# Optimization experiments

Hardware: AMD Instinct MI355X
Metric: run time of the kernel (lower is better)

## Reference

```python
import jax, jax.numpy as jnp
import numpy as np

POS_LEN = 19
SEQ = POS_LEN * POS_LEN
C = 768
H = 12
HD = C // H  # 64
FFN = 2048
L = 8
EPS = 1e-6


def make_rope():
    # 2D rotary embedding over the 19x19 board, half the freq dims for rows, half for cols.
    d_half = HD // 2          # 32
    quarter = d_half // 2     # 16
    inv_freq = 1.0 / (10000.0 ** (jnp.arange(quarter, dtype=jnp.float32) / quarter))
    pos = jnp.arange(POS_LEN, dtype=jnp.float32)
    rows = jnp.repeat(pos, POS_LEN)   # [SEQ]
    cols = jnp.tile(pos, POS_LEN)     # [SEQ]
    ang_r = rows[:, None] * inv_freq[None, :]  # [SEQ, quarter]
    ang_c = cols[:, None] * inv_freq[None, :]  # [SEQ, quarter]
    emb = jnp.concatenate([ang_r, ang_c], axis=-1)      # [SEQ, HD//2]
    emb = jnp.concatenate([emb, emb], axis=-1)          # [SEQ, HD]
    return jnp.cos(emb), jnp.sin(emb)


def rmsnorm(x, gamma):
    var = jnp.mean(jnp.square(x), axis=-1, keepdims=True)
    return x * jax.lax.rsqrt(var + EPS) * gamma


def rotate_half(x):
    a, b = jnp.split(x, 2, axis=-1)
    return jnp.concatenate([-b, a], axis=-1)


def apply_rope(x, cos, sin):
    # x: [B,S,H,HD], cos/sin: [S,HD]
    return x * cos[None, :, None, :] + rotate_half(x) * sin[None, :, None, :]


def setup_inputs() -> dict:
    key = jax.random.key(0)
    ks = jax.random.split(key, 10)
    s = 0.02
    inp = {
        "input_spatial": jax.random.normal(ks[0], (32, 22, POS_LEN, POS_LEN), jnp.float32),
        "input_global": jax.random.normal(ks[1], (32, 19), jnp.float32),
        "conv_w": jax.random.normal(ks[2], (C, 22, 3, 3), jnp.float32) * s,
        "Wg": jax.random.normal(ks[3], (19, C), jnp.float32) * s,
        "qkv_gamma": jnp.ones((L, C), jnp.float32),
        "Wqkv": jax.random.normal(ks[4], (L, C, 3 * C), jnp.float32) * s,
        "Wproj": jax.random.normal(ks[5], (L, C, C), jnp.float32) * s,
        "mlp_gamma": jnp.ones((L, C), jnp.float32),
        "Wfc1": jax.random.normal(ks[6], (L, C, 2 * FFN), jnp.float32) * s,
        "Wfc2": jax.random.normal(ks[7], (L, FFN, C), jnp.float32) * s,
        "final_gamma": jnp.ones((C,), jnp.float32),
    }
    return inp


def reference(input_spatial, input_global, conv_w, Wg, qkv_gamma, Wqkv, Wproj,
              mlp_gamma, Wfc1, Wfc2, final_gamma):
    B = input_spatial.shape[0]
    cos, sin = make_rope()
    # Stem: conv over spatial planes + broadcast global linear
    x_sp = jax.lax.conv_general_dilated(
        input_spatial, conv_w, window_strides=(1, 1), padding="SAME",
        dimension_numbers=("NCHW", "OIHW", "NCHW"))           # [B,C,19,19]
    x_g = input_global @ Wg                                       # [B,C]
    x = x_sp + x_g[:, :, None, None]
    x = x.reshape(B, C, SEQ).transpose(0, 2, 1)                   # [B,S,C]

    scale = 1.0 / jnp.sqrt(jnp.float32(HD))
    for i in range(L):
        # RMSNorm + QKV
        h = rmsnorm(x, qkv_gamma[i])
        qkv = (h @ Wqkv[i]).reshape(B, SEQ, 3, H, HD)
        q, k, v = qkv[:, :, 0], qkv[:, :, 1], qkv[:, :, 2]        # [B,S,H,HD]
        q = apply_rope(q, cos, sin)
        k = apply_rope(k, cos, sin)
        # Attention (no mask)
        scores = jnp.einsum("bshd,bthd->bhst", q, k) * scale      # [B,H,S,S]
        attn = jax.nn.softmax(scores, axis=-1)
        o = jnp.einsum("bhst,bthd->bshd", attn, v).reshape(B, SEQ, C)
        x = x + o @ Wproj[i]
        # RMSNorm + SwiGLU MLP
        h = rmsnorm(x, mlp_gamma[i])
        u = h @ Wfc1[i]                                           # [B,S,2*FFN]
        a, b = jnp.split(u, 2, axis=-1)
        x = x + (jax.nn.silu(a) * b) @ Wfc2[i]

    return rmsnorm(x, final_gamma).astype(jnp.float32)
```

## Files before the change

kernel.cpp:

```cpp
#include <hip/hip_runtime.h>
#include <hip/hip_bf16.h>
#include <math.h>

#define B_    32
#define SEQ_  361
#define C_    768
#define H_    12
#define HD_   64
#define FFN_  2048
#define L_    8
#define M_    (B_*SEQ_)
#define MPAD_ 11648
#define MBLK_ (MPAD_/128)

typedef _Float16 f16;
typedef f16  f16x8 __attribute__((ext_vector_type(8)));
typedef float f32x4 __attribute__((ext_vector_type(4)));

__global__ void bias_kernel(const float* __restrict__ inG, const float* __restrict__ Wg,
                            float* __restrict__ bias) {
  int idx = blockIdx.x * blockDim.x + threadIdx.x;
  if (idx >= B_ * C_) return;
  int b = idx / C_, c = idx - b * C_;
  float acc = 0.f;
  #pragma unroll
  for (int j = 0; j < 19; ++j) acc += inG[b * 19 + j] * Wg[j * C_ + c];
  bias[idx] = acc;
}

__global__ void rope_table_kernel(float* __restrict__ cost, float* __restrict__ sint) {
  int idx = blockIdx.x * blockDim.x + threadIdx.x;
  if (idx >= SEQ_ * 32) return;
  int s = idx / 32, j = idx - s * 32;
  float row = (float)(s / 19), col = (float)(s % 19);
  int q = (j < 16) ? j : (j - 16);
  float invf = powf(10000.f, -(float)q / 16.f);
  float ang = ((j < 16) ? row : col) * invf;
  float cv = cosf(ang), sv = sinf(ang);
  cost[s * 64 + j] = cv; cost[s * 64 + j + 32] = cv;
  sint[s * 64 + j] = sv; sint[s * 64 + j + 32] = sv;
}

__global__ __launch_bounds__(256) void conv_kernel(const float* __restrict__ inS,
    const float* __restrict__ convW, const float* __restrict__ bias,
    float* __restrict__ X) {
  __shared__ float in_l[22][441];
  __shared__ float w_l[24][198];
  int b = blockIdx.x;
  int cb = blockIdx.y * 24;
  int tid = threadIdx.x;
  for (int i = tid; i < 22 * 441; i += 256) (&in_l[0][0])[i] = 0.f;
  __syncthreads();
  for (int i = tid; i < 22 * 361; i += 256) {
    int ci = i / 361, s = i - ci * 361, r = s / 19, c = s - r * 19;
    in_l[ci][(r + 1) * 21 + (c + 1)] = inS[(size_t)(b * 22 + ci) * 361 + s];
  }
  for (int i = tid; i < 24 * 198; i += 256)
    (&w_l[0][0])[i] = convW[(size_t)cb * 198 + i];
  __syncthreads();
  for (int o = tid; o < 24 * 361; o += 256) {
    int col = o / 361, s = o - col * 361, r = s / 19, c = s - r * 19;
    float acc = bias[b * C_ + cb + col];
    const float* wr = &w_l[col][0];
    #pragma unroll
    for (int ci = 0; ci < 22; ++ci) {
      const float* ib = &in_l[ci][r * 21 + c];
      const float* wp = wr + ci * 9;
      acc += wp[0]*ib[0]  + wp[1]*ib[1]  + wp[2]*ib[2]
           + wp[3]*ib[21] + wp[4]*ib[22] + wp[5]*ib[23]
           + wp[6]*ib[42] + wp[7]*ib[43] + wp[8]*ib[44];
    }
    X[(size_t)(b * SEQ_ + s) * C_ + cb + col] = acc;
  }
}

__global__ __launch_bounds__(256) void wcvt_kernel(const float* __restrict__ W,
    f16* __restrict__ WT, int K, int N) {
  __shared__ float t[32][33];
  int n0 = blockIdx.x * 32, k0 = blockIdx.y * 32;
  size_t base = (size_t)blockIdx.z * K * N;
  int c = threadIdx.x & 31, r = threadIdx.x >> 5;
  #pragma unroll
  for (int rr = 0; rr < 32; rr += 8)
    t[r + rr][c] = W[base + (size_t)(k0 + r + rr) * N + n0 + c];
  __syncthreads();
  #pragma unroll
  for (int rr = 0; rr < 32; rr += 8)
    WT[base + (size_t)(n0 + r + rr) * K + k0 + c] = (f16)t[c][r + rr];
}

template<bool F16OUT>
__global__ __launch_bounds__(256) void rmsnorm_kernel(const float* __restrict__ X,
    const float* __restrict__ gamma, void* __restrict__ Out) {
  int row = blockIdx.x;
  const float* xp = X + (size_t)row * C_;
  int t = threadIdx.x;
  float v0 = xp[t], v1 = xp[t + 256], v2 = xp[t + 512];
  float ss = v0 * v0 + v1 * v1 + v2 * v2;
  #pragma unroll
  for (int off = 32; off > 0; off >>= 1) ss += __shfl_down(ss, off);
  __shared__ float ws4[4];
  if ((t & 63) == 0) ws4[t >> 6] = ss;
  __syncthreads();
  float tot = ws4[0] + ws4[1] + ws4[2] + ws4[3];
  float r = 1.0f / sqrtf(tot * (1.f / 768.f) + 1e-6f);
  if (F16OUT) {
    f16* op = (f16*)Out + (size_t)row * C_;
    op[t]       = (f16)(v0 * r * gamma[t]);
    op[t + 256] = (f16)(v1 * r * gamma[t + 256]);
    op[t + 512] = (f16)(v2 * r * gamma[t + 512]);
  } else {
    float* op = (float*)Out + (size_t)row * C_;
    op[t]       = v0 * r * gamma[t];
    op[t + 256] = v1 * r * gamma[t + 256];
    op[t + 512] = v2 * r * gamma[t + 512];
  }
}

template<int MODE>
__global__ __launch_bounds__(256, 2) void hgemm(const f16* __restrict__ A,
    const f16* __restrict__ BT, void* __restrict__ Cout, int N, int K) {
  __shared__ f16 As[128 * 32];
  __shared__ f16 Bs[128 * 32];
  int tid = threadIdx.x;
  int w = tid >> 6, lane = tid & 63, lo = lane & 15, hi = lane >> 4;
  int bm = blockIdx.y * 128, bn = blockIdx.x * 128;
  int wr = (w >> 1) * 64, wc = (w & 1) * 64;
  f32x4 acc[4][4] = {};
  f16x8 ra[2], rb[2];
  const f16* Abase = A  + (size_t)bm * K;
  const f16* Bbase = BT + (size_t)bn * K;

  auto loadT = [&](int kt) {
    #pragma unroll
    for (int c = 0; c < 2; ++c) {
      int id = c * 256 + tid;
      ra[c] = *(const f16x8*)(Abase + (size_t)(id >> 2) * K + kt + (id & 3) * 8);
      rb[c] = *(const f16x8*)(Bbase + (size_t)(id >> 2) * K + kt + (id & 3) * 8);
    }
  };
  auto writeT = [&]() {
    #pragma unroll
    for (int c = 0; c < 2; ++c) {
      int id = c * 256 + tid;
      int row = id >> 2, ch = id & 3;
      int off = row * 32 + ((ch ^ ((row >> 1) & 3)) << 3);
      *(f16x8*)(As + off) = ra[c];
      *(f16x8*)(Bs + off) = rb[c];
    }
  };

  loadT(0);
  for (int kt = 0; kt < K; kt += 32) {
    writeT();
    __syncthreads();
    if (kt + 32 < K) loadT(kt + 32);
    f16x8 af[4], bf[4];
    #pragma unroll
    for (int m = 0; m < 4; ++m) {
      int row = wr + m * 16 + lo;
      af[m] = *(const f16x8*)(As + row * 32 + ((hi ^ ((row >> 1) & 3)) << 3));
    }
    #pragma unroll
    for (int n = 0; n < 4; ++n) {
      int row = wc + n * 16 + lo;
      bf[n] = *(const f16x8*)(Bs + row * 32 + ((hi ^ ((row >> 1) & 3)) << 3));
    }
    #pragma unroll
    for (int m = 0; m < 4; ++m)
      #pragma unroll
      for (int n = 0; n < 4; ++n)
        acc[m][n] = __builtin_amdgcn_mfma_f32_16x16x32_f16(af[m], bf[n], acc[m][n], 0, 0, 0);
    __syncthreads();
  }

  #pragma unroll
  for (int m = 0; m < 4; ++m) {
    #pragma unroll
    for (int n = 0; n < 4; ++n) {
      #pragma unroll
      for (int r = 0; r < 4; ++r) {
        size_t off = (size_t)(bm + wr + m * 16 + hi * 4 + r) * N + bn + wc + n * 16 + lo;
        if (MODE == 0) {
          ((f16*)Cout)[off] = (f16)acc[m][n][r];
        } else {
          float* O = (float*)Cout;
          O[off] = O[off] + acc[m][n][r];
        }
      }
    }
  }
}

__global__ __launch_bounds__(256, 2) void hgemm_gate(const f16* __restrict__ A,
    const f16* __restrict__ BT, f16* __restrict__ G) {
  const int K = C_;
  __shared__ f16 As[128 * 32];
  __shared__ f16 Bs0[64 * 32];
  __shared__ f16 Bs1[64 * 32];
  int tid = threadIdx.x;
  int w = tid >> 6, lane = tid & 63, lo = lane & 15, hi = lane >> 4;
  int bm = blockIdx.y * 128, bn = blockIdx.x * 64;
  int wr = (w >> 1) * 64, wc = (w & 1) * 32;
  f32x4 accA[4][2] = {}, accB[4][2] = {};
  f16x8 ra[2], rb0, rb1;
  const f16* Abase  = A + (size_t)bm * K;
  const f16* B0base = BT + (size_t)bn * K;
  const f16* B1base = BT + (size_t)(2048 + bn) * K;

  auto loadT = [&](int kt) {
    #pragma unroll
    for (int c = 0; c < 2; ++c) {
      int id = c * 256 + tid;
      ra[c] = *(const f16x8*)(Abase + (size_t)(id >> 2) * K + kt + (id & 3) * 8);
    }
    rb0 = *(const f16x8*)(B0base + (size_t)(tid >> 2) * K + kt + (tid & 3) * 8);
    rb1 = *(const f16x8*)(B1base + (size_t)(tid >> 2) * K + kt + (tid & 3) * 8);
  };
  auto writeT = [&]() {
    #pragma unroll
    for (int c = 0; c < 2; ++c) {
      int id = c * 256 + tid;
      int row = id >> 2, ch = id & 3;
      *(f16x8*)(As + row * 32 + ((ch ^ ((row >> 1) & 3)) << 3)) = ra[c];
    }
    int row = tid >> 2, ch = tid & 3;
    int off = row * 32 + ((ch ^ ((row >> 1) & 3)) << 3);
    *(f16x8*)(Bs0 + off) = rb0;
    *(f16x8*)(Bs1 + off) = rb1;
  };

  loadT(0);
  for (int kt = 0; kt < K; kt += 32) {
    writeT();
    __syncthreads();
    if (kt + 32 < K) loadT(kt + 32);
    f16x8 af[4], b0f[2], b1f[2];
    #pragma unroll
    for (int m = 0; m < 4; ++m) {
      int row = wr + m * 16 + lo;
      af[m] = *(const f16x8*)(As + row * 32 + ((hi ^ ((row >> 1) & 3)) << 3));
    }
    #pragma unroll
    for (int n = 0; n < 2; ++n) {
      int row = wc + n * 16 + lo;
      int off = row * 32 + ((hi ^ ((row >> 1) & 3)) << 3);
      b0f[n] = *(const f16x8*)(Bs0 + off);
      b1f[n] = *(const f16x8*)(Bs1 + off);
    }
    #pragma unroll
    for (int m = 0; m < 4; ++m)
      #pragma unroll
      for (int n = 0; n < 2; ++n) {
        accA[m][n] = __builtin_amdgcn_mfma_f32_16x16x32_f16(af[m], b0f[n], accA[m][n], 0, 0, 0);
        accB[m][n] = __builtin_amdgcn_mfma_f32_16x16x32_f16(af[m], b1f[n], accB[m][n], 0, 0, 0);
      }
    __syncthreads();
  }

  #pragma unroll
  for (int m = 0; m < 4; ++m)
    #pragma unroll
    for (int n = 0; n < 2; ++n)
      #pragma unroll
      for (int r = 0; r < 4; ++r) {
        float a = accA[m][n][r], bb = accB[m][n][r];
        float g = a / (1.f + expf(-a)) * bb;
        G[(size_t)(bm + wr + m * 16 + hi * 4 + r) * 2048 + bn + wc + n * 16 + lo] = (f16)g;
      }
}

__global__ void rope_apply_kernel(f16* __restrict__ qkv,
    const float* __restrict__ cost, const float* __restrict__ sint) {
  int idx = blockIdx.x * blockDim.x + threadIdx.x;
  const int total = M_ * 2 * H_ * 32;
  if (idx >= total) return;
  int d = idx & 31;
  int rest = idx >> 5;
  int h = rest % H_; rest /= H_;
  int which = rest & 1; rest >>= 1;
  int s = rest % SEQ_;
  int b = rest / SEQ_;
  size_t base = (size_t)(b * SEQ_ + s) * (3 * C_) + which * C_ + h * 64;
  float a  = (float)qkv[base + d];
  float bb = (float)qkv[base + d + 32];
  float cv = cost[s * 64 + d], sv = sint[s * 64 + d];
  qkv[base + d]      = (f16)(a * cv - bb * sv);
  qkv[base + d + 32] = (f16)(bb * cv + a * sv);
}

__global__ __launch_bounds__(256, 2) void attn_kernel(const f16* __restrict__ qkv,
                                                      f16* __restrict__ Out) {
  __shared__ f16 Kl[64 * 64];
  __shared__ f16 Vt[64 * 72];
  __shared__ f16 Pl[4][16 * 72];
  int tid = threadIdx.x;
  int w = tid >> 6, lane = tid & 63, lo = lane & 15, hi = lane >> 4;
  int qt = blockIdx.x, h = blockIdx.y, b = blockIdx.z;
  int q0 = qt * 64 + w * 16;
  const int RS = 3 * C_;

  f16x8 qf[2];
  {
    int qrow = q0 + lo; if (qrow > 360) qrow = 360;
    const f16* qp = qkv + (size_t)(b * SEQ_ + qrow) * RS + h * 64 + hi * 8;
    qf[0] = *(const f16x8*)(qp);
    qf[1] = *(const f16x8*)(qp + 32);
  }
  f32x4 o[4] = {};
  float mrun[4], lrun[4];
  #pragma unroll
  for (int r = 0; r < 4; ++r) { mrun[r] = -INFINITY; lrun[r] = 0.f; }

  for (int kt = 0; kt < SEQ_; kt += 64) {
    #pragma unroll
    for (int c = 0; c < 2; ++c) {
      int id = c * 256 + tid;
      {
        int row = id >> 3, ch = id & 7;
        int key = kt + row; if (key > 360) key = 360;
        f16x8 kv = *(const f16x8*)(qkv + (size_t)(b * SEQ_ + key) * RS + C_ + h * 64 + ch * 8);
        *(f16x8*)(Kl + row * 64 + ((ch ^ (row & 7)) << 3)) = kv;
      }
      {
        int kk = id & 63, d0 = (id >> 6) * 8;
        int key = kt + kk; if (key > 360) key = 360;
        f16x8 vv = *(const f16x8*)(qkv + (size_t)(b * SEQ_ + key) * RS + 2 * C_ + h * 64 + d0);
        #pragma unroll
        for (int j = 0; j < 8; ++j) Vt[(d0 + j) * 72 + kk] = vv[j];
      }
    }
    __syncthreads();

    f32x4 s[4] = {};
    #pragma unroll
    for (int f = 0; f < 4; ++f) {
      int row = f * 16 + lo;
      f16x8 k0 = *(const f16x8*)(Kl + row * 64 + ((hi ^ (row & 7)) << 3));
      f16x8 k1 = *(const f16x8*)(Kl + row * 64 + (((hi + 4) ^ (row & 7)) << 3));
      s[f] = __builtin_amdgcn_mfma_f32_16x16x32_f16(qf[0], k0, s[f], 0, 0, 0);
      s[f] = __builtin_amdgcn_mfma_f32_16x16x32_f16(qf[1], k1, s[f], 0, 0, 0);
    }
    float tmax[4] = {-INFINITY, -INFINITY, -INFINITY, -INFINITY};
    #pragma unroll
    for (int f = 0; f < 4; ++f) {
      bool ok = (kt + f * 16 + lo) < SEQ_;
      #pragma unroll
      for (int r = 0; r < 4; ++r) {
        float v = ok ? s[f][r] * 0.125f : -INFINITY;
        s[f][r] = v;
        tmax[r] = fmaxf(tmax[r], v);
      }
    }
    #pragma unroll
    for (int r = 0; r < 4; ++r) {
      #pragma unroll
      for (int mk = 1; mk < 16; mk <<= 1) tmax[r] = fmaxf(tmax[r], __shfl_xor(tmax[r], mk));
    }
    float rsc[4], psum[4] = {0.f, 0.f, 0.f, 0.f};
    #pragma unroll
    for (int r = 0; r < 4; ++r) {
      float mn = fmaxf(mrun[r], tmax[r]);
      rsc[r] = expf(mrun[r] - mn);
      mrun[r] = mn;
    }
    #pragma unroll
    for (int f = 0; f < 4; ++f)
      #pragma unroll
      for (int r = 0; r < 4; ++r) {
        float p = expf(s[f][r] - mrun[r]);
        s[f][r] = p;
        psum[r] += p;
      }
    #pragma unroll
    for (int r = 0; r < 4; ++r) {
      #pragma unroll
      for (int mk = 1; mk < 16; mk <<= 1) psum[r] += __shfl_xor(psum[r], mk);
      lrun[r] = lrun[r] * rsc[r] + psum[r];
    }
    #pragma unroll
    for (int n = 0; n < 4; ++n)
      #pragma unroll
      for (int r = 0; r < 4; ++r) o[n][r] *= rsc[r];
    f16* P = &Pl[w][0];
    #pragma unroll
    for (int f = 0; f < 4; ++f)
      #pragma unroll
      for (int r = 0; r < 4; ++r)
        P[(hi * 4 + r) * 72 + f * 16 + lo] = (f16)s[f][r];
    #pragma unroll
    for (int ks = 0; ks < 2; ++ks) {
      f16x8 pa = *(const f16x8*)(P + lo * 72 + hi * 8 + ks * 32);
      #pragma unroll
      for (int n = 0; n < 4; ++n) {
        f16x8 vf = *(const f16x8*)(Vt + (n * 16 + lo) * 72 + hi * 8 + ks * 32);
        o[n] = __builtin_amdgcn_mfma_f32_16x16x32_f16(pa, vf, o[n], 0, 0, 0);
      }
    }
    __syncthreads();
  }

  #pragma unroll
  for (int r = 0; r < 4; ++r) {
    int row = q0 + hi * 4 + r;
    if (row < SEQ_) {
      float inv = 1.f / lrun[r];
      #pragma unroll
      for (int n = 0; n < 4; ++n)
        Out[(size_t)(b * SEQ_ + row) * C_ + h * 64 + n * 16 + lo] = (f16)(o[n][r] * inv);
    }
  }
}

extern "C" void kernel_launch(void* const* d_in, const int* in_sizes, int n_in,
                              void* d_out, int out_size, void* d_ws, size_t ws_size,
                              hipStream_t stream) {
  (void)in_sizes; (void)n_in; (void)out_size;
  const float* inS   = (const float*)d_in[0];
  const float* inG   = (const float*)d_in[1];
  const float* convW = (const float*)d_in[2];
  const float* Wg    = (const float*)d_in[3];
  const float* qg    = (const float*)d_in[4];
  const float* Wqkv  = (const float*)d_in[5];
  const float* Wproj = (const float*)d_in[6];
  const float* mg    = (const float*)d_in[7];
  const float* Wfc1  = (const float*)d_in[8];
  const float* Wfc2  = (const float*)d_in[9];
  const float* fg    = (const float*)d_in[10];
  float* out = (float*)d_out;

  char* p = (char*)d_ws;
  float* x    = (float*)p;            p += (size_t)MPAD_ * C_ * 4;
  float* bias = (float*)p;            p += (size_t)B_ * C_ * 4;
  float* cost = (float*)p;            p += (size_t)SEQ_ * 64 * 4;
  float* sint = (float*)p;            p += (size_t)SEQ_ * 64 * 4;
  f16*   h16  = (f16*)p;              p += (size_t)MPAD_ * C_ * 2;
  f16*   qkv16= (f16*)p;              p += (size_t)MPAD_ * 3 * C_ * 2;
  f16*   g16  = qkv16;

  const size_t sq = (size_t)3 * C_ * C_;
  const size_t sp = (size_t)C_ * C_;
  const size_t s1 = (size_t)2 * FFN_ * C_;
  const size_t s2 = (size_t)C_ * FFN_;
  const size_t per_layer = sq + sp + s1 + s2;
  size_t used_common = (size_t)(p - (char*)d_ws);
  bool upfront = ws_size >= used_common + per_layer * L_ * 2 + 1024;
  size_t mult = upfront ? (size_t)L_ : 1;
  f16* wq  = (f16*)p;
  f16* wpj = wq  + sq * mult;
  f16* w1  = wpj + sp * mult;
  f16* w2  = w1  + s1 * mult;

  bias_kernel<<<dim3((B_ * C_ + 255) / 256), 256, 0, stream>>>(inG, Wg, bias);
  rope_table_kernel<<<dim3((SEQ_ * 32 + 255) / 256), 256, 0, stream>>>(cost, sint);
  conv_kernel<<<dim3(B_, 32), 256, 0, stream>>>(inS, convW, bias, x);

  if (upfront) {
    wcvt_kernel<<<dim3(3 * C_ / 32, C_ / 32, L_), 256, 0, stream>>>(Wqkv, wq, C_, 3 * C_);
    wcvt_kernel<<<dim3(C_ / 32, C_ / 32, L_), 256, 0, stream>>>(Wproj, wpj, C_, C_);
    wcvt_kernel<<<dim3(2 * FFN_ / 32, C_ / 32, L_), 256, 0, stream>>>(Wfc1, w1, C_, 2 * FFN_);
    wcvt_kernel<<<dim3(C_ / 32, FFN_ / 32, L_), 256, 0, stream>>>(Wfc2, w2, FFN_, C_);
  }

  for (int i = 0; i < L_; ++i) {
    if (!upfront) {
      wcvt_kernel<<<dim3(3 * C_ / 32, C_ / 32, 1), 256, 0, stream>>>(Wqkv + (size_t)i * sq, wq, C_, 3 * C_);
      wcvt_kernel<<<dim3(C_ / 32, C_ / 32, 1), 256, 0, stream>>>(Wproj + (size_t)i * sp, wpj, C_, C_);
      wcvt_kernel<<<dim3(2 * FFN_ / 32, C_ / 32, 1), 256, 0, stream>>>(Wfc1 + (size_t)i * s1, w1, C_, 2 * FFN_);
      wcvt_kernel<<<dim3(C_ / 32, FFN_ / 32, 1), 256, 0, stream>>>(Wfc2 + (size_t)i * s2, w2, FFN_, C_);
    }
    const f16* Wq_i = wq  + (upfront ? (size_t)i * sq : 0);
    const f16* Wp_i = wpj + (upfront ? (size_t)i * sp : 0);
    const f16* W1_i = w1  + (upfront ? (size_t)i * s1 : 0);
    const f16* W2_i = w2  + (upfront ? (size_t)i * s2 : 0);

    rmsnorm_kernel<true><<<MPAD_, 256, 0, stream>>>(x, qg + (size_t)i * C_, h16);
    hgemm<0><<<dim3(3 * C_ / 128, MBLK_), 256, 0, stream>>>(h16, Wq_i, qkv16, 3 * C_, C_);
    rope_apply_kernel<<<dim3((M_ * 2 * H_ * 32 + 255) / 256), 256, 0, stream>>>(qkv16, cost, sint);
    attn_kernel<<<dim3(6, H_, B_), 256, 0, stream>>>(qkv16, h16);
    hgemm<1><<<dim3(C_ / 128, MBLK_), 256, 0, stream>>>(h16, Wp_i, x, C_, C_);
    rmsnorm_kernel<true><<<MPAD_, 256, 0, stream>>>(x, mg + (size_t)i * C_, h16);
    hgemm_gate<<<dim3(FFN_ / 64, MBLK_), 256, 0, stream>>>(h16, W1_i, g16);
    hgemm<1><<<dim3(C_ / 128, MBLK_), 256, 0, stream>>>(g16, W2_i, x, C_, FFN_);
  }
  rmsnorm_kernel<false><<<M_, 256, 0, stream>>>(x, fg, out);
}
```

Measured before the change: 3.666 ms.

## Use async global-to-LDS double buffering in GEMMs, fuse RoPE, convert conv to GEMM

```diff
diff --git a/kernel.cpp b/kernel.cpp
--- a/kernel.cpp
+++ b/kernel.cpp
@@ -12,10 +12,16 @@
 #define M_    (B_*SEQ_)
 #define MPAD_ 11648
 #define MBLK_ (MPAD_/128)
+#define KC_   224
 
 typedef _Float16 f16;
 typedef f16  f16x8 __attribute__((ext_vector_type(8)));
 typedef float f32x4 __attribute__((ext_vector_type(4)));
+
+#define GLDS(g, l) \
+  __builtin_amdgcn_global_load_lds( \
+      (const __attribute__((address_space(1))) void*)(g), \
+      (__attribute__((address_space(3))) void*)(l), 16, 0, 0)
 
 __global__ void bias_kernel(const float* __restrict__ inG, const float* __restrict__ Wg,
                             float* __restrict__ bias) {
@@ -41,37 +47,28 @@
   sint[s * 64 + j] = sv; sint[s * 64 + j + 32] = sv;
 }
 
-__global__ __launch_bounds__(256) void conv_kernel(const float* __restrict__ inS,
-    const float* __restrict__ convW, const float* __restrict__ bias,
-    float* __restrict__ X) {
-  __shared__ float in_l[22][441];
-  __shared__ float w_l[24][198];
-  int b = blockIdx.x;
-  int cb = blockIdx.y * 24;
-  int tid = threadIdx.x;
-  for (int i = tid; i < 22 * 441; i += 256) (&in_l[0][0])[i] = 0.f;
-  __syncthreads();
-  for (int i = tid; i < 22 * 361; i += 256) {
-    int ci = i / 361, s = i - ci * 361, r = s / 19, c = s - r * 19;
-    in_l[ci][(r + 1) * 21 + (c + 1)] = inS[(size_t)(b * 22 + ci) * 361 + s];
-  }
-  for (int i = tid; i < 24 * 198; i += 256)
-    (&w_l[0][0])[i] = convW[(size_t)cb * 198 + i];
-  __syncthreads();
-  for (int o = tid; o < 24 * 361; o += 256) {
-    int col = o / 361, s = o - col * 361, r = s / 19, c = s - r * 19;
-    float acc = bias[b * C_ + cb + col];
-    const float* wr = &w_l[col][0];
-    #pragma unroll
-    for (int ci = 0; ci < 22; ++ci) {
-      const float* ib = &in_l[ci][r * 21 + c];
-      const float* wp = wr + ci * 9;
-      acc += wp[0]*ib[0]  + wp[1]*ib[1]  + wp[2]*ib[2]
-           + wp[3]*ib[21] + wp[4]*ib[22] + wp[5]*ib[23]
-           + wp[6]*ib[42] + wp[7]*ib[43] + wp[8]*ib[44];
-    }
-    X[(size_t)(b * SEQ_ + s) * C_ + cb + col] = acc;
-  }
+__global__ void im2col_kernel(const float* __restrict__ inS, f16* __restrict__ A16) {
+  int idx = blockIdx.x * 256 + threadIdx.x;
+  if (idx >= MPAD_ * KC_) return;
+  int m = idx / KC_, k = idx - m * KC_;
+  float v = 0.f;
+  if (m < M_ && k < 198) {
+    int b = m / 361, s = m - b * 361;
+    int r = s / 19, c = s - r * 19;
+    int ci = k / 9, rem = k - ci * 9;
+    int dr = rem / 3 - 1, dc = rem - (rem / 3) * 3 - 1;
+    int rr = r + dr, cc = c + dc;
+    if (rr >= 0 && rr < 19 && cc >= 0 && cc < 19)
+      v = inS[(size_t)(b * 22 + ci) * 361 + rr * 19 + cc];
+  }
+  A16[idx] = (f16)v;
+}
+
+__global__ void wcvt_conv_kernel(const float* __restrict__ W, f16* __restrict__ WT) {
+  int idx = blockIdx.x * 256 + threadIdx.x;
+  if (idx >= 768 * KC_) return;
+  int n = idx / KC_, k = idx - n * KC_;
+  WT[idx] = (f16)(k < 198 ? W[n * 198 + k] : 0.f);
 }
 
 __global__ __launch_bounds__(256) void wcvt_kernel(const float* __restrict__ W,
@@ -118,53 +115,47 @@
 }
 
 template<int MODE>
-__global__ __launch_bounds__(256, 2) void hgemm(const f16* __restrict__ A,
-    const f16* __restrict__ BT, void* __restrict__ Cout, int N, int K) {
-  __shared__ f16 As[128 * 32];
-  __shared__ f16 Bs[128 * 32];
+__global__ __launch_bounds__(256, 3) void hgemm(const f16* __restrict__ A,
+    const f16* __restrict__ BT, void* __restrict__ Cout, const float* __restrict__ Bias,
+    const float* __restrict__ Cst, const float* __restrict__ Snt,
+    int N, int K) {
+  __shared__ f16 As[2 * 128 * 32];
+  __shared__ f16 Bs[2 * 128 * 32];
   int tid = threadIdx.x;
   int w = tid >> 6, lane = tid & 63, lo = lane & 15, hi = lane >> 4;
   int bm = blockIdx.y * 128, bn = blockIdx.x * 128;
   int wr = (w >> 1) * 64, wc = (w & 1) * 64;
   f32x4 acc[4][4] = {};
-  f16x8 ra[2], rb[2];
   const f16* Abase = A  + (size_t)bm * K;
   const f16* Bbase = BT + (size_t)bn * K;
 
-  auto loadT = [&](int kt) {
-    #pragma unroll
-    for (int c = 0; c < 2; ++c) {
-      int id = c * 256 + tid;
-      ra[c] = *(const f16x8*)(Abase + (size_t)(id >> 2) * K + kt + (id & 3) * 8);
-      rb[c] = *(const f16x8*)(Bbase + (size_t)(id >> 2) * K + kt + (id & 3) * 8);
+  int srow = lane >> 2;
+  auto stage = [&](int buf, int kt) {
+    #pragma unroll
+    for (int j = 0; j < 2; ++j) {
+      int r0 = j * 64 + w * 16;
+      int row = r0 + srow;
+      int chg = (lane & 3) ^ ((row >> 1) & 3);
+      GLDS(Abase + (size_t)row * K + kt + chg * 8, As + buf * 4096 + r0 * 32);
+      GLDS(Bbase + (size_t)row * K + kt + chg * 8, Bs + buf * 4096 + r0 * 32);
     }
   };
-  auto writeT = [&]() {
-    #pragma unroll
-    for (int c = 0; c < 2; ++c) {
-      int id = c * 256 + tid;
-      int row = id >> 2, ch = id & 3;
-      int off = row * 32 + ((ch ^ ((row >> 1) & 3)) << 3);
-      *(f16x8*)(As + off) = ra[c];
-      *(f16x8*)(Bs + off) = rb[c];
-    }
-  };
-
-  loadT(0);
+
+  stage(0, 0);
+  __syncthreads();
+  int cur = 0;
   for (int kt = 0; kt < K; kt += 32) {
-    writeT();
-    __syncthreads();
-    if (kt + 32 < K) loadT(kt + 32);
+    if (kt + 32 < K) stage(cur ^ 1, kt + 32);
     f16x8 af[4], bf[4];
     #pragma unroll
     for (int m = 0; m < 4; ++m) {
       int row = wr + m * 16 + lo;
-      af[m] = *(const f16x8*)(As + row * 32 + ((hi ^ ((row >> 1) & 3)) << 3));
+      af[m] = *(const f16x8*)(As + cur * 4096 + row * 32 + ((hi ^ ((row >> 1) & 3)) << 3));
     }
     #pragma unroll
     for (int n = 0; n < 4; ++n) {
       int row = wc + n * 16 + lo;
-      bf[n] = *(const f16x8*)(Bs + row * 32 + ((hi ^ ((row >> 1) & 3)) << 3));
+      bf[n] = *(const f16x8*)(Bs + cur * 4096 + row * 32 + ((hi ^ ((row >> 1) & 3)) << 3));
     }
     #pragma unroll
     for (int m = 0; m < 4; ++m)
@@ -172,79 +163,92 @@
       for (int n = 0; n < 4; ++n)
         acc[m][n] = __builtin_amdgcn_mfma_f32_16x16x32_f16(af[m], bf[n], acc[m][n], 0, 0, 0);
     __syncthreads();
-  }
-
+    cur ^= 1;
+  }
+
+  const bool do_rope = (MODE == 0) && (Cst != nullptr) && ((bn + wc) < 1536);
   #pragma unroll
   for (int m = 0; m < 4; ++m) {
     #pragma unroll
-    for (int n = 0; n < 4; ++n) {
-      #pragma unroll
-      for (int r = 0; r < 4; ++r) {
-        size_t off = (size_t)(bm + wr + m * 16 + hi * 4 + r) * N + bn + wc + n * 16 + lo;
-        if (MODE == 0) {
-          ((f16*)Cout)[off] = (f16)acc[m][n][r];
-        } else {
-          float* O = (float*)Cout;
-          O[off] = O[off] + acc[m][n][r];
+    for (int r = 0; r < 4; ++r) {
+      int row = bm + wr + m * 16 + hi * 4 + r;
+      if (do_rope) {
+        int s = row % 361;
+        f16* O = (f16*)Cout + (size_t)row * N + bn + wc;
+        #pragma unroll
+        for (int n = 0; n < 2; ++n) {
+          int d = n * 16 + lo;
+          float cv = Cst[s * 64 + d], sv = Snt[s * 64 + d];
+          float a = acc[m][n][r], b2 = acc[m][n + 2][r];
+          O[d]      = (f16)(a * cv - b2 * sv);
+          O[d + 32] = (f16)(b2 * cv + a * sv);
         }
-      }
-    }
-  }
-}
-
-__global__ __launch_bounds__(256, 2) void hgemm_gate(const f16* __restrict__ A,
+      } else {
+        #pragma unroll
+        for (int n = 0; n < 4; ++n) {
+          int col = bn + wc + n * 16 + lo;
+          size_t off = (size_t)row * N + col;
+          if (MODE == 0) {
+            ((f16*)Cout)[off] = (f16)acc[m][n][r];
+          } else if (MODE == 1) {
+            float* O = (float*)Cout;
+            O[off] = O[off] + acc[m][n][r];
+          } else {
+            int b = row / 361; if (b > 31) b = 31;
+            ((float*)Cout)[off] = acc[m][n][r] + Bias[b * N + col];
+          }
+        }
+      }
+    }
+  }
+}
+
+__global__ __launch_bounds__(256, 3) void hgemm_gate(const f16* __restrict__ A,
     const f16* __restrict__ BT, f16* __restrict__ G) {
   const int K = C_;
-  __shared__ f16 As[128 * 32];
-  __shared__ f16 Bs0[64 * 32];
-  __shared__ f16 Bs1[64 * 32];
+  __shared__ f16 As[2 * 128 * 32];
+  __shared__ f16 Bs0[2 * 64 * 32];
+  __shared__ f16 Bs1[2 * 64 * 32];
   int tid = threadIdx.x;
   int w = tid >> 6, lane = tid & 63, lo = lane & 15, hi = lane >> 4;
   int bm = blockIdx.y * 128, bn = blockIdx.x * 64;
   int wr = (w >> 1) * 64, wc = (w & 1) * 32;
   f32x4 accA[4][2] = {}, accB[4][2] = {};
-  f16x8 ra[2], rb0, rb1;
   const f16* Abase  = A + (size_t)bm * K;
   const f16* B0base = BT + (size_t)bn * K;
   const f16* B1base = BT + (size_t)(2048 + bn) * K;
 
-  auto loadT = [&](int kt) {
-    #pragma unroll
-    for (int c = 0; c < 2; ++c) {
-      int id = c * 256 + tid;
-      ra[c] = *(const f16x8*)(Abase + (size_t)(id >> 2) * K + kt + (id & 3) * 8);
-    }
-    rb0 = *(const f16x8*)(B0base + (size_t)(tid >> 2) * K + kt + (tid & 3) * 8);
-    rb1 = *(const f16x8*)(B1base + (size_t)(tid >> 2) * K + kt + (tid & 3) * 8);
+  int srow = lane >> 2;
+  auto stage = [&](int buf, int kt) {
+    #pragma unroll
+    for (int j = 0; j < 2; ++j) {
+      int r0 = j * 64 + w * 16;
+      int row = r0 + srow;
+      int chg = (lane & 3) ^ ((row >> 1) & 3);
+      GLDS(Abase + (size_t)row * K + kt + chg * 8, As + buf * 4096 + r0 * 32);
+    }
+    int r0 = w * 16;
+    int row = r0 + srow;
+    int chg = (lane & 3) ^ ((row >> 1) & 3);
+    GLDS(B0base + (size_t)row * K + kt + chg * 8, Bs0 + buf * 2048 + r0 * 32);
+    GLDS(B1base + (size_t)row * K + kt + chg * 8, Bs1 + buf * 2048 + r0 * 32);
   };
-  auto writeT = [&]() {
-    #pragma unroll
-    for (int c = 0; c < 2; ++c) {
-      int id = c * 256 + tid;
-      int row = id >> 2, ch = id & 3;
-      *(f16x8*)(As + row * 32 + ((ch ^ ((row >> 1) & 3)) << 3)) = ra[c];
-    }
-    int row = tid >> 2, ch = tid & 3;
-    int off = row * 32 + ((ch ^ ((row >> 1) & 3)) << 3);
-    *(f16x8*)(Bs0 + off) = rb0;
-    *(f16x8*)(Bs1 + off) = rb1;
-  };
-
-  loadT(0);
+
+  stage(0, 0);
+  __syncthreads();
+  int cur = 0;
   for (int kt = 0; kt < K; kt += 32) {
-    writeT();
-    __syncthreads();
-    if (kt + 32 < K) loadT(kt + 32);
+    if (kt + 32 < K) stage(cur ^ 1, kt + 32);
     f16x8 af[4], b0f[2], b1f[2];
     #pragma unroll
     for (int m = 0; m < 4; ++m) {
       int row = wr + m * 16 + lo;
-      af[m] = *(const f16x8*)(As + row * 32 + ((hi ^ ((row >> 1) & 3)) << 3));
+      af[m] = *(const f16x8*)(As + cur * 4096 + row * 32 + ((hi ^ ((row >> 1) & 3)) << 3));
     }
     #pragma unroll
     for (int n = 0; n < 2; ++n) {
       int row = wc + n * 16 + lo;
-      int off = row * 32 + ((hi ^ ((row >> 1) & 3)) << 3);
+      int off = cur * 2048 + row * 32 + ((hi ^ ((row >> 1) & 3)) << 3);
       b0f[n] = *(const f16x8*)(Bs0 + off);
       b1f[n] = *(const f16x8*)(Bs1 + off);
     }
@@ -256,6 +260,7 @@
         accB[m][n] = __builtin_amdgcn_mfma_f32_16x16x32_f16(af[m], b1f[n], accB[m][n], 0, 0, 0);
       }
     __syncthreads();
+    cur ^= 1;
   }
 
   #pragma unroll
@@ -268,25 +273,6 @@
         float g = a / (1.f + expf(-a)) * bb;
         G[(size_t)(bm + wr + m * 16 + hi * 4 + r) * 2048 + bn + wc + n * 16 + lo] = (f16)g;
       }
-}
-
-__global__ void rope_apply_kernel(f16* __restrict__ qkv,
-    const float* __restrict__ cost, const float* __restrict__ sint) {
-  int idx = blockIdx.x * blockDim.x + threadIdx.x;
-  const int total = M_ * 2 * H_ * 32;
-  if (idx >= total) return;
-  int d = idx & 31;
-  int rest = idx >> 5;
-  int h = rest % H_; rest /= H_;
-  int which = rest & 1; rest >>= 1;
-  int s = rest % SEQ_;
-  int b = rest / SEQ_;
-  size_t base = (size_t)(b * SEQ_ + s) * (3 * C_) + which * C_ + h * 64;
-  float a  = (float)qkv[base + d];
-  float bb = (float)qkv[base + d + 32];
-  float cv = cost[s * 64 + d], sv = sint[s * 64 + d];
-  qkv[base + d]      = (f16)(a * cv - bb * sv);
-  qkv[base + d + 32] = (f16)(bb * cv + a * sv);
 }
 
 __global__ __launch_bounds__(256, 2) void attn_kernel(const f16* __restrict__ qkv,
@@ -436,6 +422,8 @@
   float* sint = (float*)p;            p += (size_t)SEQ_ * 64 * 4;
   f16*   h16  = (f16*)p;              p += (size_t)MPAD_ * C_ * 2;
   f16*   qkv16= (f16*)p;              p += (size_t)MPAD_ * 3 * C_ * 2;
+  f16*   a16c = (f16*)p;              p += (size_t)MPAD_ * KC_ * 2;
+  f16*   wc16 = (f16*)p;              p += (size_t)C_ * KC_ * 2;
   f16*   g16  = qkv16;
 
   const size_t sq = (size_t)3 * C_ * C_;
@@ -453,7 +441,9 @@
 
   bias_kernel<<<dim3((B_ * C_ + 255) / 256), 256, 0, stream>>>(inG, Wg, bias);
   rope_table_kernel<<<dim3((SEQ_ * 32 + 255) / 256), 256, 0, stream>>>(cost, sint);
-  conv_kernel<<<dim3(B_, 32), 256, 0, stream>>>(inS, convW, bias, x);
+  im2col_kernel<<<dim3((MPAD_ * KC_ + 255) / 256), 256, 0, stream>>>(inS, a16c);
+  wcvt_conv_kernel<<<dim3((768 * KC_ + 255) / 256), 256, 0, stream>>>(convW, wc16);
+  hgemm<2><<<dim3(C_ / 128, MBLK_), 256, 0, stream>>>(a16c, wc16, x, bias, nullptr, nullptr, C_, KC_);
 
   if (upfront) {
     wcvt_kernel<<<dim3(3 * C_ / 32, C_ / 32, L_), 256, 0, stream>>>(Wqkv, wq, C_, 3 * C_);
@@ -475,13 +465,15 @@
     const f16* W2_i = w2  + (upfront ? (size_t)i * s2 : 0);
 
     rmsnorm_kernel<true><<<MPAD_, 256, 0, stream>>>(x, qg + (size_t)i * C_, h16);
-    hgemm<0><<<dim3(3 * C_ / 128, MBLK_), 256, 0, stream>>>(h16, Wq_i, qkv16, 3 * C_, C_);
-    rope_apply_kernel<<<dim3((M_ * 2 * H_ * 32 + 255) / 256), 256, 0, stream>>>(qkv16, cost, sint);
+    hgemm<0><<<dim3(3 * C_ / 128, MBLK_), 256, 0, stream>>>(
+        h16, Wq_i, qkv16, nullptr, cost, sint, 3 * C_, C_);
     attn_kernel<<<dim3(6, H_, B_), 256, 0, stream>>>(qkv16, h16);
-    hgemm<1><<<dim3(C_ / 128, MBLK_), 256, 0, stream>>>(h16, Wp_i, x, C_, C_);
+    hgemm<1><<<dim3(C_ / 128, MBLK_), 256, 0, stream>>>(
+        h16, Wp_i, x, nullptr, nullptr, nullptr, C_, C_);
     rmsnorm_kernel<true><<<MPAD_, 256, 0, stream>>>(x, mg + (size_t)i * C_, h16);
     hgemm_gate<<<dim3(FFN_ / 64, MBLK_), 256, 0, stream>>>(h16, W1_i, g16);
-    hgemm<1><<<dim3(C_ / 128, MBLK_), 256, 0, stream>>>(g16, W2_i, x, C_, FFN_);
+    hgemm<1><<<dim3(C_ / 128, MBLK_), 256, 0, stream>>>(
+        g16, W2_i, x, nullptr, nullptr, nullptr, C_, FFN_);
   }
   rmsnorm_kernel<false><<<M_, 256, 0, stream>>>(x, fg, out);
 }
```

Result: faster. 3.172 ms (-13.5%).
